# Optimization experiments

Measured on AMD Instinct MI355X. Metric: run time of the kernel, lower is better.

The kernel has to match this reference:

```python
import jax, jax.numpy as jnp
import numpy as np

TEMP = 0.5
A_LC = 1.0


def setup_inputs() -> dict:
    key = jax.random.key(0)
    kx, kl = jax.random.split(key)
    b, nviews, d = 8192, 2, 128
    x = jax.random.normal(kx, (b, nviews, d), dtype=jnp.float32)
    labels = jax.random.randint(kl, (b,), 0, 10, dtype=jnp.int64)
    return {"x": x, "labels": labels}


def reference(x, labels):
    # x: [b, 2, d]; labels: [b]
    # Defaults: log_first=True, old_lnew=False, detect_noise=False,
    # pos_in_denom=False, K=-1, noise_rate=0, a_spread=0, lc_norm=False.
    # Only view pair (ii=1, jj=0) contributes; pairs = 1.
    vi = x[:, 1, :]  # [b, d]
    vj = x[:, 0, :]  # [b, d]
    num = jnp.einsum('bd,cd->bc', vi, vj) / TEMP  # [b, b]

    pos = labels[:, None] == labels[None, :]  # [b, b] same-class (incl. self)
    neg = ~pos

    # logsumexp over each row's negatives (stable, masked)
    neg_num = jnp.where(neg, num, -jnp.inf)
    L_neg = jax.nn.logsumexp(neg_num, axis=1)  # [b]

    # denominator[i] = sum_{p in pos(i)} logsumexp([num[i,p], num[i, negs(i)]])
    #               = sum_{p in pos(i)} logaddexp(num[i,p], L_neg[i])
    lae = jnp.logaddexp(num, L_neg[:, None])  # [b, b]
    denominator = jnp.where(pos, lae, 0.0).sum(axis=1)  # [b]
    numerator = -jnp.where(pos, num, 0.0).sum(axis=1)   # [b]

    div_factor = pos.sum(axis=1).astype(num.dtype)  # |pos(i)| >= 1
    log_prob = numerator + denominator
    a = A_LC * log_prob / div_factor
    pairs = 1.0
    return a.mean() / pairs
```

## Files before the change

### kernel.cpp

```cpp
#include <hip/hip_runtime.h>
#include <hip/hip_bf16.h>
#include <math.h>

#define DDIM 128
#define JS 32
#define ROWS_BLK 128
#define NGMAX 16
#define NCLS 10
#define TMAX 16
#define CMAX 128.0f
#define LOG2E 1.44269504f
#define LN2F 0.69314718f
#define MBIAS (-CMAX * LOG2E)

typedef __attribute__((ext_vector_type(8))) short short8;
typedef __attribute__((ext_vector_type(4))) float f32x4;

__device__ __forceinline__ ushort f2bf(float f) {
    union { float f; unsigned u; } v; v.f = f;
    unsigned r = (v.u + 0x7FFFu + ((v.u >> 16) & 1u)) >> 16;
    return (ushort)r;
}

__device__ __forceinline__ void gload_lds16(const ushort* g, ushort* l) {
    __builtin_amdgcn_global_load_lds(
        (const __attribute__((address_space(1))) unsigned int*)g,
        (__attribute__((address_space(3))) unsigned int*)l,
        16, 0, 0);
}

__global__ __launch_bounds__(256) void convert_kernel(
    const float* __restrict__ x, ushort* __restrict__ vi, ushort* __restrict__ vj, int B)
{
    int t = blockIdx.x * 256 + threadIdx.x;
    int r = t >> 5;
    int k4 = (t & 31) * 4;
    if (r >= B) return;
    float4 a = *reinterpret_cast<const float4*>(x + (size_t)r * 256 + DDIM + k4);
    float4 b = *reinterpret_cast<const float4*>(x + (size_t)r * 256 + k4);
    ushort4 ua, ub;
    ua.x = f2bf(a.x * 2.0f); ua.y = f2bf(a.y * 2.0f); ua.z = f2bf(a.z * 2.0f); ua.w = f2bf(a.w * 2.0f);
    ub.x = f2bf(b.x); ub.y = f2bf(b.y); ub.z = f2bf(b.z); ub.w = f2bf(b.w);
    *reinterpret_cast<ushort4*>(vi + (size_t)r * DDIM + k4) = ua;
    *reinterpret_cast<ushort4*>(vj + (size_t)r * DDIM + k4) = ub;
}

__global__ __launch_bounds__(1024) void build_index_kernel(
    const int* __restrict__ labels, int* __restrict__ idx, int* __restrict__ counts, int B)
{
    const int c = blockIdx.x;
    const int tid = threadIdx.x;
    const int wave = tid >> 6, lane = tid & 63;
    __shared__ int base;
    __shared__ int wsum[16];
    if (tid == 0) base = 0;
    __syncthreads();
    for (int start = 0; start < B; start += 1024) {
        bool m = (labels[start + tid] == c);
        unsigned long long mask = __ballot(m);
        int lrank = __popcll(mask & ((1ull << lane) - 1ull));
        if (lane == 0) wsum[wave] = __popcll(mask);
        __syncthreads();
        int wbase = 0, total = 0;
        #pragma unroll
        for (int w = 0; w < 16; ++w) {
            if (w < wave) wbase += wsum[w];
            total += wsum[w];
        }
        int b0 = base;
        __syncthreads();
        if (m) idx[c * B + b0 + wbase + lrank] = start + tid;
        if (tid == 0) base = b0 + total;
        __syncthreads();
    }
    if (tid == 0) counts[c] = base;
}

__global__ __launch_bounds__(256, 4) void pass1_kernel(
    const ushort* __restrict__ vi, const ushort* __restrict__ vj,
    const int* __restrict__ labels, float* __restrict__ os, int B)
{
    __shared__ ushort lbuf[4][16 * DDIM];

    const int tid = threadIdx.x;
    const int wave = tid >> 6, lane = tid & 63;
    const int col16 = lane & 15, grp = lane >> 4;
    const int nbr = B / ROWS_BLK;
    const int rb = blockIdx.x % nbr;
    const int chunk = blockIdx.x / nbr;
    const int ri0 = rb * ROWS_BLK + wave * 32;
    const int jchunk = B / JS;
    const int j0 = chunk * jchunk;
    const int NG = jchunk / 16;

    short8 afrag[8];
    #pragma unroll
    for (int h = 0; h < 2; ++h)
        #pragma unroll
        for (int ks = 0; ks < 4; ++ks)
            afrag[h * 4 + ks] = *reinterpret_cast<const short8*>(
                vi + (size_t)(ri0 + h * 16 + col16) * DDIM + ks * 32 + grp * 8);

    int rl[8];
    float s[8];
    #pragma unroll
    for (int r = 0; r < 8; ++r) {
        int row = ri0 + (r >> 2) * 16 + grp * 4 + (r & 3);
        rl[r] = labels[row];
        s[r] = 0.0f;
    }

    int cl[NGMAX];
    #pragma unroll
    for (int g = 0; g < NGMAX; ++g)
        cl[g] = labels[j0 + g * 16 + col16];

    const int lrow  = wave * 4 + (lane >> 4);
    const int lslot = lane & 15;
    const int gslot = lslot ^ (lrow & 7);

    auto STAGE = [&](int g) {
        int jb = j0 + g * 16;
        gload_lds16(vj + (size_t)(jb + lrow) * DDIM + gslot * 8,
                    &lbuf[g & 3][(wave * 4) * DDIM]);
    };
    auto COMP = [&](int g) {
        const ushort* buf = lbuf[g & 3];
        int clg = cl[g];
        short8 bfrag[4];
        #pragma unroll
        for (int ks = 0; ks < 4; ++ks) {
            int p = (ks * 4 + grp) ^ (col16 & 7);
            bfrag[ks] = *reinterpret_cast<const short8*>(&buf[col16 * DDIM + p * 8]);
        }
        #pragma unroll
        for (int h = 0; h < 2; ++h) {
            f32x4 acc = (f32x4){0.f, 0.f, 0.f, 0.f};
            #pragma unroll
            for (int ks = 0; ks < 4; ++ks)
                acc = __builtin_amdgcn_mfma_f32_16x16x32_bf16(afrag[h * 4 + ks], bfrag[ks], acc, 0, 0, 0);
            #pragma unroll
            for (int rr = 0; rr < 4; ++rr) {
                int r = h * 4 + rr;
                float e = exp2f(fmaf(acc[rr], LOG2E, MBIAS));
                e = (clg == rl[r]) ? 0.0f : e;
                s[r] += e;
            }
        }
    };

    STAGE(0);
    STAGE(1);
    for (int g = 0; g < NG; ++g) {
        if (g + 2 < NG) {
            STAGE(g + 2);
            asm volatile("s_waitcnt vmcnt(2)" ::: "memory");
        } else if (g + 1 < NG) {
            asm volatile("s_waitcnt vmcnt(1)" ::: "memory");
        } else {
            asm volatile("s_waitcnt vmcnt(0)" ::: "memory");
        }
        asm volatile("s_barrier" ::: "memory");
        COMP(g);
    }

    #pragma unroll
    for (int r = 0; r < 8; ++r) {
        for (int off = 8; off; off >>= 1) s[r] += __shfl_xor(s[r], off);
        if (col16 == 0) {
            int row = ri0 + (r >> 2) * 16 + grp * 4 + (r & 3);
            os[chunk * B + row] = s[r];
        }
    }
}

__global__ __launch_bounds__(256) void merge_sneg_kernel(
    const float* __restrict__ os, float* __restrict__ sneg, int B)
{
    int i = blockIdx.x * 256 + threadIdx.x;
    if (i >= B) return;
    float s = 0.0f;
    #pragma unroll
    for (int h = 0; h < JS; ++h) s += os[h * B + i];
    sneg[i] = s;
}

__global__ __launch_bounds__(256) void pass2_kernel(
    const ushort* __restrict__ vi, const ushort* __restrict__ vj,
    const int* __restrict__ idx, const int* __restrict__ counts,
    const float* __restrict__ sneg,
    float* __restrict__ p, int B)
{
    const int c  = blockIdx.x / TMAX;
    const int rt = blockIdx.x % TMAX;
    const int qt = blockIdx.y;
    const int n  = counts[c];
    if (rt * 64 >= n || qt * 64 >= n) return;
    const int tid = threadIdx.x;
    const int wave = tid >> 6, lane = tid & 63;
    const int col16 = lane & 15, grp = lane >> 4;
    const int* cidx = idx + c * B;

    for (int rt2 = rt; rt2 * 64 < n; rt2 += TMAX) {
        const int ri0 = rt2 * 64 + wave * 16;
        int aslot = ri0 + col16;
        int aid = cidx[aslot < n ? aslot : n - 1];
        short8 afrag[4];
        #pragma unroll
        for (int ks = 0; ks < 4; ++ks)
            afrag[ks] = *reinterpret_cast<const short8*>(
                vi + (size_t)aid * DDIM + ks * 32 + grp * 8);

        bool rv[4];
        int rid[4];
        float sn[4], s[4];
        #pragma unroll
        for (int r = 0; r < 4; ++r) {
            int slot = ri0 + grp * 4 + r;
            rv[r] = slot < n;
            rid[r] = cidx[slot < n ? slot : n - 1];
            sn[r] = sneg[rid[r]];
            s[r] = 0.0f;
        }

        for (int qt2 = qt; qt2 * 64 < n; qt2 += TMAX) {
            const int jb = qt2 * 64;
            bool jv[4];
            int cid[4];
            f32x4 acc[4];
            #pragma unroll
            for (int cg = 0; cg < 4; ++cg) {
                int slot = jb + cg * 16 + col16;
                jv[cg] = slot < n;
                cid[cg] = cidx[slot < n ? slot : n - 1];
                acc[cg] = (f32x4){0.f, 0.f, 0.f, 0.f};
            }
            #pragma unroll
            for (int cg = 0; cg < 4; ++cg) {
                #pragma unroll
                for (int ks = 0; ks < 4; ++ks) {
                    short8 bfrag = *reinterpret_cast<const short8*>(
                        vj + (size_t)cid[cg] * DDIM + ks * 32 + grp * 8);
                    acc[cg] = __builtin_amdgcn_mfma_f32_16x16x32_bf16(afrag[ks], bfrag, acc[cg], 0, 0, 0);
                }
            }
            #pragma unroll
            for (int r = 0; r < 4; ++r) {
                #pragma unroll
                for (int cg = 0; cg < 4; ++cg) {
                    float v = acc[cg][r];
                    float e = exp2f(fmaf(v, LOG2E, MBIAS));
                    float d = fmaf(__log2f(e + sn[r] + 1e-38f), LN2F, CMAX) - v;
                    if (jv[cg]) s[r] += d;
                }
            }
        }

        #pragma unroll
        for (int r = 0; r < 4; ++r) {
            for (int off = 8; off; off >>= 1) s[r] += __shfl_xor(s[r], off);
            if (col16 == 0 && rv[r]) p[qt * B + rid[r]] = s[r];
        }
    }
}

__global__ __launch_bounds__(256) void merge_pass2_kernel(
    const int* __restrict__ labels, const int* __restrict__ counts,
    const float* __restrict__ p, double* __restrict__ part, int B)
{
    int i = blockIdx.x * 256 + threadIdx.x;
    int n = counts[labels[i]];
    int ntq = (n + 63) >> 6;
    if (ntq > TMAX) ntq = TMAX;
    float s = 0.0f;
    for (int q = 0; q < ntq; ++q) s += p[q * B + i];
    double contrib = (double)(s / (float)n);
    __shared__ double red[256];
    red[threadIdx.x] = contrib;
    __syncthreads();
    for (int off = 128; off; off >>= 1) {
        if (threadIdx.x < off) red[threadIdx.x] += red[threadIdx.x + off];
        __syncthreads();
    }
    if (threadIdx.x == 0) part[blockIdx.x] = red[0];
}

__global__ __launch_bounds__(64) void finalize_kernel(
    const double* __restrict__ part, float* __restrict__ out, int nparts, int B)
{
    __shared__ double red[64];
    double v = (threadIdx.x < nparts) ? part[threadIdx.x] : 0.0;
    red[threadIdx.x] = v;
    __syncthreads();
    for (int off = 32; off; off >>= 1) {
        if (threadIdx.x < off) red[threadIdx.x] += red[threadIdx.x + off];
        __syncthreads();
    }
    if (threadIdx.x == 0) out[0] = (float)(red[0] / (double)B);
}

extern "C" void kernel_launch(void* const* d_in, const int* in_sizes, int n_in,
                              void* d_out, int out_size, void* d_ws, size_t ws_size,
                              hipStream_t stream) {
    const float* x      = (const float*)d_in[0];
    const int*   labels = (const int*)d_in[1];
    int B = in_sizes[1];
    float* out = (float*)d_out;

    ushort* vi     = (ushort*)d_ws;
    ushort* vj     = vi + (size_t)B * DDIM;
    float*  os     = (float*)(vj + (size_t)B * DDIM);
    float*  p      = os;
    float*  sneg   = os + (size_t)JS * B;
    int*    idx    = (int*)(sneg + B);
    int*    counts = idx + (size_t)NCLS * B;
    double* part   = (double*)(counts + 64);

    convert_kernel<<<dim3(B * 32 / 256), dim3(256), 0, stream>>>(x, vi, vj, B);
    build_index_kernel<<<dim3(NCLS), dim3(1024), 0, stream>>>(labels, idx, counts, B);

    int nbr = B / ROWS_BLK;
    pass1_kernel<<<dim3(nbr * JS), dim3(256), 0, stream>>>(vi, vj, labels, os, B);
    merge_sneg_kernel<<<dim3((B + 255) / 256), dim3(256), 0, stream>>>(os, sneg, B);
    pass2_kernel<<<dim3(NCLS * TMAX, TMAX), dim3(256), 0, stream>>>(vi, vj, idx, counts, sneg, p, B);
    merge_pass2_kernel<<<dim3(B / 256), dim3(256), 0, stream>>>(labels, counts, p, part, B);
    finalize_kernel<<<dim3(1), dim3(64), 0, stream>>>(part, out, B / 256, B);
}
```

Before: 85.46 us.

## Widen pass1 column groups, halve j-splits, fold sneg merge into pass2

Pass1 now stages 32 columns per step into a three-buffer LDS ring with one stage of lookahead, down from 16 columns and two stages. The j-split count drops from 32 to 16, so the number of pass1 blocks halves and each block does more work. Column labels are staged in LDS instead of held in registers. The separate merge_sneg kernel is removed and pass2 sums the 16 partial negative sums per row inline, saving a launch at the cost of redundant reads in pass2. The workspace layout is updated so p no longer aliases os.

```diff
diff --git a/kernel.cpp b/kernel.cpp
--- a/kernel.cpp
+++ b/kernel.cpp
@@ -3,9 +3,10 @@
 #include <math.h>
 
 #define DDIM 128
-#define JS 32
+#define JS 16
+#define GCOLS 32
+#define NG 16
 #define ROWS_BLK 128
-#define NGMAX 16
 #define NCLS 10
 #define TMAX 16
 #define CMAX 128.0f
@@ -80,7 +81,8 @@
     const ushort* __restrict__ vi, const ushort* __restrict__ vj,
     const int* __restrict__ labels, float* __restrict__ os, int B)
 {
-    __shared__ ushort lbuf[4][16 * DDIM];
+    __shared__ ushort lbuf[3][GCOLS * DDIM];
+    __shared__ int lbl_s[JS == 0 ? 1 : (GCOLS * NG)];
 
     const int tid = threadIdx.x;
     const int wave = tid >> 6, lane = tid & 63;
@@ -91,7 +93,6 @@
     const int ri0 = rb * ROWS_BLK + wave * 32;
     const int jchunk = B / JS;
     const int j0 = chunk * jchunk;
-    const int NG = jchunk / 16;
 
     short8 afrag[8];
     #pragma unroll
@@ -110,53 +111,62 @@
         s[r] = 0.0f;
     }
 
-    int cl[NGMAX];
-    #pragma unroll
-    for (int g = 0; g < NGMAX; ++g)
-        cl[g] = labels[j0 + g * 16 + col16];
-
-    const int lrow  = wave * 4 + (lane >> 4);
+    int2 lb = *reinterpret_cast<const int2*>(labels + j0 + 2 * tid);
+    lbl_s[2 * tid]     = lb.x;
+    lbl_s[2 * tid + 1] = lb.y;
+
+    const int crow  = wave * 4 + (lane >> 4);
     const int lslot = lane & 15;
-    const int gslot = lslot ^ (lrow & 7);
 
     auto STAGE = [&](int g) {
-        int jb = j0 + g * 16;
-        gload_lds16(vj + (size_t)(jb + lrow) * DDIM + gslot * 8,
-                    &lbuf[g & 3][(wave * 4) * DDIM]);
+        int jb = j0 + g * GCOLS;
+        ushort* base = lbuf[g % 3];
+        #pragma unroll
+        for (int i = 0; i < 2; ++i) {
+            int c = i * 16 + crow;
+            int slot = lslot ^ (c & 7);
+            gload_lds16(vj + (size_t)(jb + c) * DDIM + slot * 8,
+                        base + (i * 16 + wave * 4) * DDIM);
+        }
     };
     auto COMP = [&](int g) {
-        const ushort* buf = lbuf[g & 3];
-        int clg = cl[g];
-        short8 bfrag[4];
-        #pragma unroll
-        for (int ks = 0; ks < 4; ++ks) {
-            int p = (ks * 4 + grp) ^ (col16 & 7);
-            bfrag[ks] = *reinterpret_cast<const short8*>(&buf[col16 * DDIM + p * 8]);
-        }
-        #pragma unroll
-        for (int h = 0; h < 2; ++h) {
-            f32x4 acc = (f32x4){0.f, 0.f, 0.f, 0.f};
-            #pragma unroll
-            for (int ks = 0; ks < 4; ++ks)
-                acc = __builtin_amdgcn_mfma_f32_16x16x32_bf16(afrag[h * 4 + ks], bfrag[ks], acc, 0, 0, 0);
-            #pragma unroll
-            for (int rr = 0; rr < 4; ++rr) {
-                int r = h * 4 + rr;
-                float e = exp2f(fmaf(acc[rr], LOG2E, MBIAS));
-                e = (clg == rl[r]) ? 0.0f : e;
-                s[r] += e;
+        const ushort* buf = lbuf[g % 3];
+        #pragma unroll
+        for (int cg = 0; cg < 2; ++cg) {
+            int clg = lbl_s[g * GCOLS + cg * 16 + col16];
+            short8 bfrag[4];
+            #pragma unroll
+            for (int ks = 0; ks < 4; ++ks) {
+                int p = (ks * 4 + grp) ^ (col16 & 7);
+                bfrag[ks] = *reinterpret_cast<const short8*>(
+                    &buf[(cg * 16 + col16) * DDIM + p * 8]);
+            }
+            #pragma unroll
+            for (int h = 0; h < 2; ++h) {
+                f32x4 acc = (f32x4){0.f, 0.f, 0.f, 0.f};
+                #pragma unroll
+                for (int ks = 0; ks < 4; ++ks)
+                    acc = __builtin_amdgcn_mfma_f32_16x16x32_bf16(afrag[h * 4 + ks], bfrag[ks], acc, 0, 0, 0);
+                #pragma unroll
+                for (int rr = 0; rr < 4; ++rr) {
+                    int r = h * 4 + rr;
+                    float e = exp2f(fmaf(acc[rr], LOG2E, MBIAS));
+                    e = (clg == rl[r]) ? 0.0f : e;
+                    s[r] += e;
+                }
             }
         }
     };
 
+    asm volatile("s_waitcnt vmcnt(0) lgkmcnt(0)" ::: "memory");
+    __syncthreads();
+
     STAGE(0);
-    STAGE(1);
+    #pragma unroll
     for (int g = 0; g < NG; ++g) {
-        if (g + 2 < NG) {
-            STAGE(g + 2);
+        if (g + 1 < NG) {
+            STAGE(g + 1);
             asm volatile("s_waitcnt vmcnt(2)" ::: "memory");
-        } else if (g + 1 < NG) {
-            asm volatile("s_waitcnt vmcnt(1)" ::: "memory");
         } else {
             asm volatile("s_waitcnt vmcnt(0)" ::: "memory");
         }
@@ -174,21 +184,10 @@
     }
 }
 
-__global__ __launch_bounds__(256) void merge_sneg_kernel(
-    const float* __restrict__ os, float* __restrict__ sneg, int B)
-{
-    int i = blockIdx.x * 256 + threadIdx.x;
-    if (i >= B) return;
-    float s = 0.0f;
-    #pragma unroll
-    for (int h = 0; h < JS; ++h) s += os[h * B + i];
-    sneg[i] = s;
-}
-
 __global__ __launch_bounds__(256) void pass2_kernel(
     const ushort* __restrict__ vi, const ushort* __restrict__ vj,
     const int* __restrict__ idx, const int* __restrict__ counts,
-    const float* __restrict__ sneg,
+    const float* __restrict__ os,
     float* __restrict__ p, int B)
 {
     const int c  = blockIdx.x / TMAX;
@@ -219,7 +218,10 @@
             int slot = ri0 + grp * 4 + r;
             rv[r] = slot < n;
             rid[r] = cidx[slot < n ? slot : n - 1];
-            sn[r] = sneg[rid[r]];
+            float acc = 0.0f;
+            #pragma unroll
+            for (int h = 0; h < JS; ++h) acc += os[h * B + rid[r]];
+            sn[r] = acc;
             s[r] = 0.0f;
         }
 
@@ -310,9 +312,8 @@
     ushort* vi     = (ushort*)d_ws;
     ushort* vj     = vi + (size_t)B * DDIM;
     float*  os     = (float*)(vj + (size_t)B * DDIM);
-    float*  p      = os;
-    float*  sneg   = os + (size_t)JS * B;
-    int*    idx    = (int*)(sneg + B);
+    float*  p      = os + (size_t)JS * B;
+    int*    idx    = (int*)(p + (size_t)TMAX * B);
     int*    counts = idx + (size_t)NCLS * B;
     double* part   = (double*)(counts + 64);
 
@@ -321,8 +322,7 @@
 
     int nbr = B / ROWS_BLK;
     pass1_kernel<<<dim3(nbr * JS), dim3(256), 0, stream>>>(vi, vj, labels, os, B);
-    merge_sneg_kernel<<<dim3((B + 255) / 256), dim3(256), 0, stream>>>(os, sneg, B);
-    pass2_kernel<<<dim3(NCLS * TMAX, TMAX), dim3(256), 0, stream>>>(vi, vj, idx, counts, sneg, p, B);
+    pass2_kernel<<<dim3(NCLS * TMAX, TMAX), dim3(256), 0, stream>>>(vi, vj, idx, counts, os, p, B);
     merge_pass2_kernel<<<dim3(B / 256), dim3(256), 0, stream>>>(labels, counts, p, part, B);
     finalize_kernel<<<dim3(1), dim3(64), 0, stream>>>(part, out, B / 256, B);
 }
```

After: 211.2 us. 147% more time.
